# Kernel optimization log

Measured on AMD Instinct MI355X. Metric: run time of the kernel, lower is better.

## Reference

```python
import jax, jax.numpy as jnp
import numpy as np


def _conv1x1(x, w, b):
    # x: [B,C,H,W], w: [O,C], b: [O] -> [B,O,H,W]
    return jnp.einsum('bchw,oc->bohw', x, w) + b[None, :, None, None]


def setup_inputs() -> dict:
    key = jax.random.key(0)
    ks = jax.random.split(key, 5)
    B, C, H, W = 4, 256, 64, 64
    C2 = C // 2
    scale = 0.02  # keep attention logits in a sane range
    return {
        'x': jax.random.normal(ks[0], (B, C, H, W), dtype=jnp.float32),
        'w_theta': jax.random.normal(ks[1], (C2, C), dtype=jnp.float32) * scale,
        'b_theta': jnp.zeros((C2,), dtype=jnp.float32),
        'w_phi': jax.random.normal(ks[2], (C2, C), dtype=jnp.float32) * scale,
        'b_phi': jnp.zeros((C2,), dtype=jnp.float32),
        'w_g': jax.random.normal(ks[3], (C2, C), dtype=jnp.float32) * scale,
        'b_g': jnp.zeros((C2,), dtype=jnp.float32),
        'w_out': jax.random.normal(ks[4], (C, C2), dtype=jnp.float32) * scale,
        'b_out': jnp.zeros((C,), dtype=jnp.float32),
    }


def reference(x, w_theta, b_theta, w_phi, b_phi, w_g, b_g, w_out, b_out):
    B, C, H, W = x.shape
    C2 = C // 2
    N = H * W
    theta = _conv1x1(x, w_theta, b_theta).reshape(B, C2, N)  # [B,C2,N]
    phi = _conv1x1(x, w_phi, b_phi).reshape(B, C2, N)        # [B,C2,N]
    g = _conv1x1(x, w_g, b_g).reshape(B, C2, N)              # [B,C2,N]
    # non-local attention: scores[b,m,n] = theta[b,:,m] . phi[b,:,n]
    scores = jnp.einsum('bcm,bcn->bmn', theta, phi)          # [B,N,N]
    attn = jax.nn.softmax(scores, axis=-1)                   # [B,N,N]
    # output = g @ attn^T : out[b,c,m] = sum_n g[b,c,n] * attn[b,m,n]
    out = jnp.einsum('bcn,bmn->bcm', g, attn)                # [B,C2,N]
    out = out.reshape(B, C2, H, W)
    return x + _conv1x1(out, w_out, b_out)
```

## Files before the change

kernel.cpp:

```cpp
#include <hip/hip_runtime.h>
#include <hip/hip_bf16.h>

#define B_  4
#define C_  256
#define C2_ 128
#define N_  4096
#define LOG2E 1.4426950408889634f

typedef unsigned short u16;
typedef __attribute__((ext_vector_type(8))) short bf16x8;
typedef __attribute__((ext_vector_type(4))) short s16x4;
typedef __attribute__((ext_vector_type(4))) float f32x4;

static __device__ __forceinline__ u16 f2bf(float f) {
    return __builtin_bit_cast(u16, __float2bfloat16(f));
}
static __device__ __forceinline__ float bf2f(u16 u) {
    return __bfloat162float(__builtin_bit_cast(__hip_bfloat16, u));
}
static __device__ __forceinline__ bf16x8 cvt8(const float* p) {
    u16 t[8];
#pragma unroll
    for (int j = 0; j < 8; ++j) t[j] = f2bf(p[j]);
    return *(const bf16x8*)t;
}
static __device__ __forceinline__ bf16x8 lds8(const u16* p) {
    s16x4 lo = *(const s16x4*)p;
    s16x4 hi = *(const s16x4*)(p + 4);
    return __builtin_shufflevector(lo, hi, 0, 1, 2, 3, 4, 5, 6, 7);
}

__global__ __launch_bounds__(256) void prep_kernel(
    const float* __restrict__ wt, const float* __restrict__ wp,
    const float* __restrict__ wg, const float* __restrict__ wo,
    u16* __restrict__ Wb, u16* __restrict__ Wob) {
    int g = (blockIdx.x * 256 + threadIdx.x) * 8;
    const float* src;
    u16* dst;
    if (g < 3 * 32768) {
        int mat = g >> 15;
        src = (mat == 0 ? wt : mat == 1 ? wp : wg) + (g & 32767);
        dst = Wb + g;
    } else {
        src = wo + (g & 32767);
        dst = Wob + (g & 32767);
    }
    float w8[8];
    *(float4*)&w8[0] = *(const float4*)src;
    *(float4*)&w8[4] = *(const float4*)(src + 4);
    *(bf16x8*)dst = cvt8(w8);
}

#define XW 268

__global__ __launch_bounds__(256, 2) void projx_kernel(
    const float* __restrict__ x, const u16* __restrict__ Wb,
    const float* __restrict__ b_theta, const float* __restrict__ b_phi,
    const float* __restrict__ b_g,
    u16* __restrict__ Q, u16* __restrict__ K, u16* __restrict__ V) {
    __shared__ __align__(16) u16 XTs[64][XW];
    u16 (*Vt)[72] = (u16(*)[72])XTs;

    int bid = blockIdx.x;
    int h   = bid >> 8;
    int r2  = bid & 255;
    int b   = r2 >> 6;
    int n0  = (r2 & 63) * 64;
    int tid = threadIdx.x;
    int wave = tid >> 6, lane = tid & 63, quad = (lane >> 4) & 3, l16 = lane & 15;

#pragma unroll
    for (int it = 0; it < 8; ++it) {
        int idx = it * 256 + tid;
        int q = idx & 15, p = idx >> 4;
        const float* r0 = x + ((size_t)b * C_ + 2 * p) * N_ + n0 + 4 * q;
        float4 v0 = *(const float4*)r0;
        float4 v1 = *(const float4*)(r0 + N_);
        const float* f0 = (const float*)&v0;
        const float* f1 = (const float*)&v1;
#pragma unroll
        for (int j = 0; j < 4; ++j) {
            unsigned pk = (unsigned)f2bf(f0[j]) | ((unsigned)f2bf(f1[j]) << 16);
            *(unsigned*)&XTs[4 * q + j][2 * p] = pk;
        }
    }
    __syncthreads();

    bf16x8 af[8];
#pragma unroll
    for (int ks = 0; ks < 8; ++ks)
        af[ks] = lds8(&XTs[wave * 16 + l16][ks * 32 + quad * 8]);
    __syncthreads();

    const float* biases[3] = { b_theta, b_phi, b_g };

#pragma unroll
    for (int mat = 0; mat < 3; ++mat) {
        const float* bias = biases[mat];
        f32x4 acc[4];
#pragma unroll
        for (int i = 0; i < 4; ++i) acc[i] = (f32x4){0.f, 0.f, 0.f, 0.f};

#pragma unroll
        for (int ct = 0; ct < 4; ++ct) {
            const u16* wrow = Wb + mat * 32768 +
                              (size_t)(h * 64 + ct * 16 + l16) * 256 + quad * 8;
            bf16x8 bfr[8];
#pragma unroll
            for (int ks = 0; ks < 8; ++ks)
                bfr[ks] = *(const bf16x8*)(wrow + ks * 32);
#pragma unroll
            for (int ks = 0; ks < 8; ++ks)
                acc[ct] = __builtin_amdgcn_mfma_f32_16x16x32_bf16(
                    af[ks], bfr[ks], acc[ct], 0, 0, 0);
        }

        if (mat < 2) {
            u16* dst = mat == 0 ? Q : K;
            float scl = mat == 0 ? LOG2E : 1.0f;
#pragma unroll
            for (int ct = 0; ct < 4; ++ct) {
                int c2 = h * 64 + ct * 16 + l16;
                float bb = bias[c2];
#pragma unroll
                for (int r = 0; r < 4; ++r) {
                    int n = n0 + wave * 16 + quad * 4 + r;
                    dst[((size_t)b * N_ + n) * C2_ + c2] =
                        f2bf((acc[ct][r] + bb) * scl);
                }
            }
        } else {
#pragma unroll
            for (int ct = 0; ct < 4; ++ct) {
                int c2 = h * 64 + ct * 16 + l16;
                float bb = bias[c2];
#pragma unroll
                for (int r = 0; r < 4; ++r)
                    Vt[ct * 16 + l16][wave * 16 + quad * 4 + r] =
                        f2bf(acc[ct][r] + bb);
            }
        }
    }
    __syncthreads();

#pragma unroll
    for (int it = 0; it < 2; ++it) {
        int idx = it * 256 + tid;
        int row = idx >> 3, n8 = (idx & 7) * 8;
        *(uint4*)(V + ((size_t)b * C2_ + h * 64 + row) * N_ + n0 + n8) =
            *(const uint4*)&Vt[row][n8];
    }
}

#define KS_LD 140
#define VS_LD 76
#define PS_LD 68

__global__ __launch_bounds__(256, 2) void attn_kernel(
    const u16* __restrict__ Q, const u16* __restrict__ K,
    const u16* __restrict__ V, u16* __restrict__ AO,
    u16* __restrict__ Opb, float* __restrict__ lsum, int nsplit) {
    const int BM = 128, BN = 64, D = C2_;
    const int per = B_ * (N_ / BM);
    int s    = blockIdx.x / per;
    int r0   = blockIdx.x % per;
    int b    = r0 / (N_ / BM);
    int m0   = (r0 % (N_ / BM)) * BM;
    int tid  = threadIdx.x;
    int wave = tid >> 6, lane = tid & 63, quad = (lane >> 4) & 3, l16 = lane & 15;

    __shared__ __align__(16) u16 Ks[BN][KS_LD];
    __shared__ __align__(16) u16 Vs[C2_][VS_LD];
    __shared__ __align__(16) u16 Psb[4][32][PS_LD];
    u16* Ps = &Psb[wave][0][0];

    bf16x8 qf[2][4];
#pragma unroll
    for (int ms = 0; ms < 2; ++ms) {
        const u16* qp = Q + ((size_t)b * N_ + m0 + wave * 32 + ms * 16 + l16) * D;
#pragma unroll
        for (int kk = 0; kk < 4; ++kk)
            qf[ms][kk] = *(const bf16x8*)(qp + kk * 32 + quad * 8);
    }

    float l_r[2][4] = {{0.f, 0.f, 0.f, 0.f}, {0.f, 0.f, 0.f, 0.f}};
    f32x4 o_acc[2][8];
#pragma unroll
    for (int ms = 0; ms < 2; ++ms)
#pragma unroll
        for (int i = 0; i < 8; ++i) o_acc[ms][i] = (f32x4){0.f, 0.f, 0.f, 0.f};

    const int tiles = N_ / BN;
    const int base = tiles / nsplit, rem = tiles % nsplit;
    const int t0 = s * base + (s < rem ? s : rem);
    const int cnt = base + (s < rem ? 1 : 0);
    const int nt0 = t0 * BN, nt1 = (t0 + cnt) * BN;

    for (int nt = nt0; nt < nt1; nt += BN) {
        const u16* kp = K + ((size_t)b * N_ + nt) * D;
#pragma unroll
        for (int it = 0; it < 4; ++it) {
            int idx = it * 256 + tid;
            int row = idx >> 4, col = (idx & 15) * 8;
            uint4 raw = *(const uint4*)(kp + row * D + col);
            *(uint2*)&Ks[row][col]     = make_uint2(raw.x, raw.y);
            *(uint2*)&Ks[row][col + 4] = make_uint2(raw.z, raw.w);
        }
#pragma unroll
        for (int it = 0; it < 4; ++it) {
            int idx = it * 256 + tid;
            int row = idx >> 3, col = (idx & 7) * 8;
            uint4 raw = *(const uint4*)(V + ((size_t)b * C2_ + row) * N_ + nt + col);
            *(uint2*)&Vs[row][col]     = make_uint2(raw.x, raw.y);
            *(uint2*)&Vs[row][col + 4] = make_uint2(raw.z, raw.w);
        }
        __syncthreads();

#pragma unroll
        for (int nn = 0; nn < 4; ++nn) {
            f32x4 a0 = (f32x4){0.f, 0.f, 0.f, 0.f};
            f32x4 a1 = (f32x4){0.f, 0.f, 0.f, 0.f};
#pragma unroll
            for (int kk = 0; kk < 4; ++kk) {
                bf16x8 kf = lds8(&Ks[nn * 16 + l16][kk * 32 + quad * 8]);
                a0 = __builtin_amdgcn_mfma_f32_16x16x32_bf16(qf[0][kk], kf, a0, 0, 0, 0);
                a1 = __builtin_amdgcn_mfma_f32_16x16x32_bf16(qf[1][kk], kf, a1, 0, 0, 0);
            }
#pragma unroll
            for (int r = 0; r < 4; ++r) {
                float p0 = __builtin_amdgcn_exp2f(a0[r]);
                float p1 = __builtin_amdgcn_exp2f(a1[r]);
                l_r[0][r] += p0;
                l_r[1][r] += p1;
                Ps[(quad * 4 + r) * PS_LD + nn * 16 + l16]        = f2bf(p0);
                Ps[(16 + quad * 4 + r) * PS_LD + nn * 16 + l16]   = f2bf(p1);
            }
        }

#pragma unroll
        for (int ks = 0; ks < 2; ++ks) {
            bf16x8 pf0 = lds8(Ps + l16 * PS_LD + ks * 32 + quad * 8);
            bf16x8 pf1 = lds8(Ps + (16 + l16) * PS_LD + ks * 32 + quad * 8);
#pragma unroll
            for (int cs = 0; cs < 8; ++cs) {
                bf16x8 vf = lds8(&Vs[cs * 16 + l16][ks * 32 + quad * 8]);
                o_acc[0][cs] = __builtin_amdgcn_mfma_f32_16x16x32_bf16(pf0, vf, o_acc[0][cs], 0, 0, 0);
                o_acc[1][cs] = __builtin_amdgcn_mfma_f32_16x16x32_bf16(pf1, vf, o_acc[1][cs], 0, 0, 0);
            }
        }
        __syncthreads();
    }

#pragma unroll
    for (int ms = 0; ms < 2; ++ms)
#pragma unroll
        for (int r = 0; r < 4; ++r) {
            l_r[ms][r] += __shfl_xor(l_r[ms][r], 1);
            l_r[ms][r] += __shfl_xor(l_r[ms][r], 2);
            l_r[ms][r] += __shfl_xor(l_r[ms][r], 4);
            l_r[ms][r] += __shfl_xor(l_r[ms][r], 8);
        }

    if (Opb) {
#pragma unroll
        for (int ms = 0; ms < 2; ++ms) {
#pragma unroll
            for (int cs = 0; cs < 8; ++cs)
#pragma unroll
                for (int r = 0; r < 4; ++r) {
                    size_t row = (size_t)s * (B_ * N_) + (size_t)b * N_ +
                                 m0 + wave * 32 + ms * 16 + quad * 4 + r;
                    Opb[row * C2_ + cs * 16 + l16] = f2bf(o_acc[ms][cs][r]);
                }
            if (l16 == 0)
#pragma unroll
                for (int r = 0; r < 4; ++r) {
                    size_t row = (size_t)s * (B_ * N_) + (size_t)b * N_ +
                                 m0 + wave * 32 + ms * 16 + quad * 4 + r;
                    lsum[row] = l_r[ms][r];
                }
        }
    } else {
#pragma unroll
        for (int ms = 0; ms < 2; ++ms)
#pragma unroll
            for (int cs = 0; cs < 8; ++cs)
#pragma unroll
                for (int r = 0; r < 4; ++r) {
                    float v = o_acc[ms][cs][r] / l_r[ms][r];
                    AO[((size_t)b * N_ + m0 + wave * 32 + ms * 16 + quad * 4 + r) * C2_ +
                       cs * 16 + l16] = f2bf(v);
                }
    }
}

#define OW 140

__global__ __launch_bounds__(256, 4) void outproj_kernel(
    const float* __restrict__ x, const u16* __restrict__ Opb,
    const float* __restrict__ lsum, const u16* __restrict__ AO,
    const u16* __restrict__ Wob, const float* __restrict__ b_out,
    float* __restrict__ y, int nsplit) {
    __shared__ __align__(16) u16 As[64][OW];
    __shared__ float Ls[64];
    int bid = blockIdx.x;
    int per_b = (C_ / 64) * (N_ / 64);
    int b   = bid / per_b;
    int rem = bid % per_b;
    int c0  = (rem / (N_ / 64)) * 64;
    int n0  = (rem % (N_ / 64)) * 64;
    int tid = threadIdx.x;
    int wave = tid >> 6, lane = tid & 63, quad = (lane >> 4) & 3, l16 = lane & 15;

    bf16x8 af[4];
#pragma unroll
    for (int kk = 0; kk < 4; ++kk)
        af[kk] = *(const bf16x8*)(Wob + (size_t)(c0 + wave * 16 + l16) * C2_ +
                                  kk * 32 + quad * 8);

    if (nsplit > 1) {
        if (tid < 64) {
            float L = 0.f;
            for (int s = 0; s < nsplit; ++s)
                L += lsum[(size_t)s * (B_ * N_) + (size_t)b * N_ + n0 + tid];
            Ls[tid] = 1.f / L;
        }
        __syncthreads();
#pragma unroll
        for (int it = 0; it < 4; ++it) {
            int idx = it * 256 + tid;
            int n = idx >> 4, c8 = (idx & 15) * 8;
            float a[8] = {0.f, 0.f, 0.f, 0.f, 0.f, 0.f, 0.f, 0.f};
            for (int s = 0; s < nsplit; ++s) {
                const u16* op = Opb +
                    ((size_t)s * (B_ * N_) + (size_t)b * N_ + n0 + n) * C2_ + c8;
                uint4 raw = *(const uint4*)op;
                const u16* rp = (const u16*)&raw;
#pragma unroll
                for (int j = 0; j < 8; ++j) a[j] += bf2f(rp[j]);
            }
            float inv = Ls[n];
            u16 o[8];
#pragma unroll
            for (int j = 0; j < 8; ++j) o[j] = f2bf(a[j] * inv);
            *(s16x4*)&As[n][c8]     = *(const s16x4*)&o[0];
            *(s16x4*)&As[n][c8 + 4] = *(const s16x4*)&o[4];
        }
    } else {
#pragma unroll
        for (int it = 0; it < 4; ++it) {
            int idx = it * 256 + tid;
            int n = idx >> 4, c8 = (idx & 15) * 8;
            uint4 raw = *(const uint4*)(AO + ((size_t)b * N_ + n0 + n) * C2_ + c8);
            *(uint2*)&As[n][c8]     = make_uint2(raw.x, raw.y);
            *(uint2*)&As[n][c8 + 4] = make_uint2(raw.z, raw.w);
        }
    }
    __syncthreads();

    f32x4 acc[4];
#pragma unroll
    for (int i = 0; i < 4; ++i) acc[i] = (f32x4){0.f, 0.f, 0.f, 0.f};

#pragma unroll
    for (int nn = 0; nn < 4; ++nn)
#pragma unroll
        for (int kk = 0; kk < 4; ++kk) {
            bf16x8 bf = lds8(&As[nn * 16 + l16][kk * 32 + quad * 8]);
            acc[nn] = __builtin_amdgcn_mfma_f32_16x16x32_bf16(af[kk], bf, acc[nn], 0, 0, 0);
        }

    int cw = c0 + wave * 16;
    float bo[4];
#pragma unroll
    for (int r = 0; r < 4; ++r) bo[r] = b_out[cw + quad * 4 + r];

#pragma unroll
    for (int nn = 0; nn < 4; ++nn)
#pragma unroll
        for (int r = 0; r < 4; ++r) {
            int c = cw + quad * 4 + r;
            size_t off = ((size_t)b * C_ + c) * N_ + n0 + nn * 16 + l16;
            y[off] = x[off] + bo[r] + acc[nn][r];
        }
}

extern "C" void kernel_launch(void* const* d_in, const int* in_sizes, int n_in,
                              void* d_out, int out_size, void* d_ws, size_t ws_size,
                              hipStream_t stream) {
    const float* x       = (const float*)d_in[0];
    const float* w_theta = (const float*)d_in[1];
    const float* b_theta = (const float*)d_in[2];
    const float* w_phi   = (const float*)d_in[3];
    const float* b_phi   = (const float*)d_in[4];
    const float* w_g     = (const float*)d_in[5];
    const float* b_g     = (const float*)d_in[6];
    const float* w_out   = (const float*)d_in[7];
    const float* b_out   = (const float*)d_in[8];
    float* y = (float*)d_out;

    const size_t SZ = (size_t)B_ * N_ * C2_;
    u16* Q   = (u16*)d_ws;
    u16* K   = Q + SZ;
    u16* V   = K + SZ;
    u16* Wb  = V + SZ;
    u16* Wob = Wb + 3 * 32768;
    char* dyn = (char*)(Wob + 32768);
    size_t fixedB = (3 * SZ + 4 * 32768) * 2;

    size_t perS = SZ * 2 + (size_t)B_ * N_ * 4;

    int S;
    if      (ws_size >= fixedB + 4 * perS) S = 4;
    else if (ws_size >= fixedB + 2 * perS) S = 2;
    else                                   S = 1;

    u16*   AO  = (u16*)dyn;
    u16*   Opb = nullptr;
    float* ls  = nullptr;
    if (S > 1) {
        Opb = (u16*)dyn;
        ls  = (float*)(Opb + (size_t)S * SZ);
    }

    prep_kernel<<<64, 256, 0, stream>>>(w_theta, w_phi, w_g, w_out, Wb, Wob);
    projx_kernel<<<B_ * (N_ / 64) * 2, 256, 0, stream>>>(
        x, Wb, b_theta, b_phi, b_g, Q, K, V);
    attn_kernel<<<B_ * (N_ / 128) * S, 256, 0, stream>>>(Q, K, V, AO, Opb, ls, S);
    outproj_kernel<<<B_ * (C_ / 64) * (N_ / 64), 256, 0, stream>>>(
        x, Opb, ls, AO, Wob, b_out, y, S);
}
```

Before: 168.9 us.

## Split projection into transpose+GEMM kernels, separate split combine, widen LDS loads

Adds a separate kernel that transposes x into bf16 [B,N,C], so the projection kernel reads A-fragments straight from global memory and each block handles one matrix and half its channels. The split-K combine moves out of outproj into its own kernel, and outproj now reads AO directly from global memory instead of staging it through LDS. In the attention kernel, LDS padding shrinks to +8, staging uses single 16-byte stores and reads, and all score MFMAs finish before the exp phase. The goal is more parallelism and fewer redundant x reads. In exchange it adds an extra bf16 copy of x, two more kernel launches, and possible LDS bank conflicts from the new padding.

```diff
diff --git a/kernel.cpp b/kernel.cpp
--- a/kernel.cpp
+++ b/kernel.cpp
@@ -9,7 +9,6 @@
 
 typedef unsigned short u16;
 typedef __attribute__((ext_vector_type(8))) short bf16x8;
-typedef __attribute__((ext_vector_type(4))) short s16x4;
 typedef __attribute__((ext_vector_type(4))) float f32x4;
 
 static __device__ __forceinline__ u16 f2bf(float f) {
@@ -23,11 +22,6 @@
 #pragma unroll
     for (int j = 0; j < 8; ++j) t[j] = f2bf(p[j]);
     return *(const bf16x8*)t;
-}
-static __device__ __forceinline__ bf16x8 lds8(const u16* p) {
-    s16x4 lo = *(const s16x4*)p;
-    s16x4 hi = *(const s16x4*)(p + 4);
-    return __builtin_shufflevector(lo, hi, 0, 1, 2, 3, 4, 5, 6, 7);
 }
 
 __global__ __launch_bounds__(256) void prep_kernel(
@@ -51,29 +45,18 @@
     *(bf16x8*)dst = cvt8(w8);
 }
 
-#define XW 268
-
-__global__ __launch_bounds__(256, 2) void projx_kernel(
-    const float* __restrict__ x, const u16* __restrict__ Wb,
-    const float* __restrict__ b_theta, const float* __restrict__ b_phi,
-    const float* __restrict__ b_g,
-    u16* __restrict__ Q, u16* __restrict__ K, u16* __restrict__ V) {
-    __shared__ __align__(16) u16 XTs[64][XW];
-    u16 (*Vt)[72] = (u16(*)[72])XTs;
-
+__global__ __launch_bounds__(256) void xpose_kernel(
+    const float* __restrict__ x, u16* __restrict__ XT) {
+    __shared__ __align__(16) u16 Ts[64][72];
     int bid = blockIdx.x;
-    int h   = bid >> 8;
-    int r2  = bid & 255;
-    int b   = r2 >> 6;
-    int n0  = (r2 & 63) * 64;
+    int b = bid >> 8, rem = bid & 255;
+    int c0 = (rem >> 6) * 64, n0 = (rem & 63) * 64;
     int tid = threadIdx.x;
-    int wave = tid >> 6, lane = tid & 63, quad = (lane >> 4) & 3, l16 = lane & 15;
-
-#pragma unroll
-    for (int it = 0; it < 8; ++it) {
+#pragma unroll
+    for (int it = 0; it < 2; ++it) {
         int idx = it * 256 + tid;
         int q = idx & 15, p = idx >> 4;
-        const float* r0 = x + ((size_t)b * C_ + 2 * p) * N_ + n0 + 4 * q;
+        const float* r0 = x + ((size_t)b * C_ + c0 + 2 * p) * N_ + n0 + 4 * q;
         float4 v0 = *(const float4*)r0;
         float4 v1 = *(const float4*)(r0 + N_);
         const float* f0 = (const float*)&v0;
@@ -81,80 +64,94 @@
 #pragma unroll
         for (int j = 0; j < 4; ++j) {
             unsigned pk = (unsigned)f2bf(f0[j]) | ((unsigned)f2bf(f1[j]) << 16);
-            *(unsigned*)&XTs[4 * q + j][2 * p] = pk;
+            *(unsigned*)&Ts[4 * q + j][2 * p] = pk;
         }
     }
     __syncthreads();
-
-    bf16x8 af[8];
-#pragma unroll
-    for (int ks = 0; ks < 8; ++ks)
-        af[ks] = lds8(&XTs[wave * 16 + l16][ks * 32 + quad * 8]);
-    __syncthreads();
-
-    const float* biases[3] = { b_theta, b_phi, b_g };
-
-#pragma unroll
-    for (int mat = 0; mat < 3; ++mat) {
-        const float* bias = biases[mat];
-        f32x4 acc[4];
-#pragma unroll
-        for (int i = 0; i < 4; ++i) acc[i] = (f32x4){0.f, 0.f, 0.f, 0.f};
-
-#pragma unroll
-        for (int ct = 0; ct < 4; ++ct) {
-            const u16* wrow = Wb + mat * 32768 +
-                              (size_t)(h * 64 + ct * 16 + l16) * 256 + quad * 8;
-            bf16x8 bfr[8];
-#pragma unroll
-            for (int ks = 0; ks < 8; ++ks)
-                bfr[ks] = *(const bf16x8*)(wrow + ks * 32);
-#pragma unroll
-            for (int ks = 0; ks < 8; ++ks)
-                acc[ct] = __builtin_amdgcn_mfma_f32_16x16x32_bf16(
-                    af[ks], bfr[ks], acc[ct], 0, 0, 0);
-        }
-
-        if (mat < 2) {
-            u16* dst = mat == 0 ? Q : K;
-            float scl = mat == 0 ? LOG2E : 1.0f;
-#pragma unroll
-            for (int ct = 0; ct < 4; ++ct) {
-                int c2 = h * 64 + ct * 16 + l16;
-                float bb = bias[c2];
-#pragma unroll
-                for (int r = 0; r < 4; ++r) {
-                    int n = n0 + wave * 16 + quad * 4 + r;
-                    dst[((size_t)b * N_ + n) * C2_ + c2] =
-                        f2bf((acc[ct][r] + bb) * scl);
-                }
-            }
-        } else {
-#pragma unroll
-            for (int ct = 0; ct < 4; ++ct) {
-                int c2 = h * 64 + ct * 16 + l16;
-                float bb = bias[c2];
-#pragma unroll
-                for (int r = 0; r < 4; ++r)
-                    Vt[ct * 16 + l16][wave * 16 + quad * 4 + r] =
-                        f2bf(acc[ct][r] + bb);
-            }
-        }
-    }
-    __syncthreads();
-
 #pragma unroll
     for (int it = 0; it < 2; ++it) {
         int idx = it * 256 + tid;
-        int row = idx >> 3, n8 = (idx & 7) * 8;
-        *(uint4*)(V + ((size_t)b * C2_ + h * 64 + row) * N_ + n0 + n8) =
-            *(const uint4*)&Vt[row][n8];
-    }
-}
-
-#define KS_LD 140
-#define VS_LD 76
-#define PS_LD 68
+        int row = idx >> 3, ch = (idx & 7) * 8;
+        *(uint4*)(XT + ((size_t)(b * N_ + n0 + row)) * C_ + c0 + ch) =
+            *(const uint4*)&Ts[row][ch];
+    }
+}
+
+__global__ __launch_bounds__(256, 2) void projx_kernel(
+    const u16* __restrict__ XT, const u16* __restrict__ Wb,
+    const float* __restrict__ b_theta, const float* __restrict__ b_phi,
+    const float* __restrict__ b_g,
+    u16* __restrict__ Q, u16* __restrict__ K, u16* __restrict__ V) {
+    __shared__ __align__(16) u16 Vt[64][72];
+
+    int bid = blockIdx.x;
+    int nt  = bid & 255;
+    int cm  = bid >> 8;
+    int mat = cm >> 1, h = cm & 1;
+    int b   = nt >> 6;
+    int n0  = (nt & 63) * 64;
+    int tid = threadIdx.x;
+    int wave = tid >> 6, lane = tid & 63, quad = (lane >> 4) & 3, l16 = lane & 15;
+
+    const u16* xrow = XT + ((size_t)(b * N_ + n0 + wave * 16 + l16)) * C_ + quad * 8;
+    bf16x8 af[8];
+#pragma unroll
+    for (int ks = 0; ks < 8; ++ks)
+        af[ks] = *(const bf16x8*)(xrow + ks * 32);
+
+    const float* bias = mat == 0 ? b_theta : mat == 1 ? b_phi : b_g;
+
+    f32x4 acc[4];
+#pragma unroll
+    for (int i = 0; i < 4; ++i) acc[i] = (f32x4){0.f, 0.f, 0.f, 0.f};
+
+#pragma unroll
+    for (int ct = 0; ct < 4; ++ct) {
+        const u16* wrow = Wb + mat * 32768 +
+                          (size_t)(h * 64 + ct * 16 + l16) * 256 + quad * 8;
+        bf16x8 bfr[8];
+#pragma unroll
+        for (int ks = 0; ks < 8; ++ks)
+            bfr[ks] = *(const bf16x8*)(wrow + ks * 32);
+#pragma unroll
+        for (int ks = 0; ks < 8; ++ks)
+            acc[ct] = __builtin_amdgcn_mfma_f32_16x16x32_bf16(
+                af[ks], bfr[ks], acc[ct], 0, 0, 0);
+    }
+
+    if (mat < 2) {
+        u16* dst = mat == 0 ? Q : K;
+        float scl = mat == 0 ? LOG2E : 1.0f;
+#pragma unroll
+        for (int ct = 0; ct < 4; ++ct) {
+            int c2 = h * 64 + ct * 16 + l16;
+            float bb = bias[c2];
+#pragma unroll
+            for (int r = 0; r < 4; ++r) {
+                int n = n0 + wave * 16 + quad * 4 + r;
+                dst[((size_t)b * N_ + n) * C2_ + c2] =
+                    f2bf((acc[ct][r] + bb) * scl);
+            }
+        }
+    } else {
+#pragma unroll
+        for (int ct = 0; ct < 4; ++ct) {
+            int c2l = ct * 16 + l16;
+            float bb = bias[h * 64 + c2l];
+#pragma unroll
+            for (int r = 0; r < 4; ++r)
+                Vt[c2l][wave * 16 + quad * 4 + r] = f2bf(acc[ct][r] + bb);
+        }
+        __syncthreads();
+#pragma unroll
+        for (int it = 0; it < 2; ++it) {
+            int idx = it * 256 + tid;
+            int row = idx >> 3, n8 = (idx & 7) * 8;
+            *(uint4*)(V + ((size_t)b * C2_ + h * 64 + row) * N_ + n0 + n8) =
+                *(const uint4*)&Vt[row][n8];
+        }
+    }
+}
 
 __global__ __launch_bounds__(256, 2) void attn_kernel(
     const u16* __restrict__ Q, const u16* __restrict__ K,
@@ -169,9 +166,9 @@
     int tid  = threadIdx.x;
     int wave = tid >> 6, lane = tid & 63, quad = (lane >> 4) & 3, l16 = lane & 15;
 
-    __shared__ __align__(16) u16 Ks[BN][KS_LD];
-    __shared__ __align__(16) u16 Vs[C2_][VS_LD];
-    __shared__ __align__(16) u16 Psb[4][32][PS_LD];
+    __shared__ __align__(16) u16 Ks[BN][D + 8];
+    __shared__ __align__(16) u16 Vs[D][BN + 8];
+    __shared__ __align__(16) u16 Psb[4][32][BN + 8];
     u16* Ps = &Psb[wave][0][0];
 
     bf16x8 qf[2][4];
@@ -202,48 +199,50 @@
         for (int it = 0; it < 4; ++it) {
             int idx = it * 256 + tid;
             int row = idx >> 4, col = (idx & 15) * 8;
-            uint4 raw = *(const uint4*)(kp + row * D + col);
-            *(uint2*)&Ks[row][col]     = make_uint2(raw.x, raw.y);
-            *(uint2*)&Ks[row][col + 4] = make_uint2(raw.z, raw.w);
+            *(uint4*)&Ks[row][col] = *(const uint4*)(kp + row * D + col);
         }
 #pragma unroll
         for (int it = 0; it < 4; ++it) {
             int idx = it * 256 + tid;
             int row = idx >> 3, col = (idx & 7) * 8;
-            uint4 raw = *(const uint4*)(V + ((size_t)b * C2_ + row) * N_ + nt + col);
-            *(uint2*)&Vs[row][col]     = make_uint2(raw.x, raw.y);
-            *(uint2*)&Vs[row][col + 4] = make_uint2(raw.z, raw.w);
+            *(uint4*)&Vs[row][col] =
+                *(const uint4*)(V + ((size_t)b * C2_ + row) * N_ + nt + col);
         }
         __syncthreads();
 
+        f32x4 sc[2][4];
 #pragma unroll
         for (int nn = 0; nn < 4; ++nn) {
             f32x4 a0 = (f32x4){0.f, 0.f, 0.f, 0.f};
             f32x4 a1 = (f32x4){0.f, 0.f, 0.f, 0.f};
 #pragma unroll
             for (int kk = 0; kk < 4; ++kk) {
-                bf16x8 kf = lds8(&Ks[nn * 16 + l16][kk * 32 + quad * 8]);
+                bf16x8 kf = *(const bf16x8*)&Ks[nn * 16 + l16][kk * 32 + quad * 8];
                 a0 = __builtin_amdgcn_mfma_f32_16x16x32_bf16(qf[0][kk], kf, a0, 0, 0, 0);
                 a1 = __builtin_amdgcn_mfma_f32_16x16x32_bf16(qf[1][kk], kf, a1, 0, 0, 0);
             }
-#pragma unroll
-            for (int r = 0; r < 4; ++r) {
-                float p0 = __builtin_amdgcn_exp2f(a0[r]);
-                float p1 = __builtin_amdgcn_exp2f(a1[r]);
-                l_r[0][r] += p0;
-                l_r[1][r] += p1;
-                Ps[(quad * 4 + r) * PS_LD + nn * 16 + l16]        = f2bf(p0);
-                Ps[(16 + quad * 4 + r) * PS_LD + nn * 16 + l16]   = f2bf(p1);
-            }
-        }
+            sc[0][nn] = a0;
+            sc[1][nn] = a1;
+        }
+
+#pragma unroll
+        for (int ms = 0; ms < 2; ++ms)
+#pragma unroll
+            for (int nn = 0; nn < 4; ++nn)
+#pragma unroll
+                for (int r = 0; r < 4; ++r) {
+                    float p = __builtin_amdgcn_exp2f(sc[ms][nn][r]);
+                    l_r[ms][r] += p;
+                    Ps[(ms * 16 + quad * 4 + r) * (BN + 8) + nn * 16 + l16] = f2bf(p);
+                }
 
 #pragma unroll
         for (int ks = 0; ks < 2; ++ks) {
-            bf16x8 pf0 = lds8(Ps + l16 * PS_LD + ks * 32 + quad * 8);
-            bf16x8 pf1 = lds8(Ps + (16 + l16) * PS_LD + ks * 32 + quad * 8);
+            bf16x8 pf0 = *(const bf16x8*)&Ps[(l16) * (BN + 8) + ks * 32 + quad * 8];
+            bf16x8 pf1 = *(const bf16x8*)&Ps[(16 + l16) * (BN + 8) + ks * 32 + quad * 8];
 #pragma unroll
             for (int cs = 0; cs < 8; ++cs) {
-                bf16x8 vf = lds8(&Vs[cs * 16 + l16][ks * 32 + quad * 8]);
+                bf16x8 vf = *(const bf16x8*)&Vs[cs * 16 + l16][ks * 32 + quad * 8];
                 o_acc[0][cs] = __builtin_amdgcn_mfma_f32_16x16x32_bf16(pf0, vf, o_acc[0][cs], 0, 0, 0);
                 o_acc[1][cs] = __builtin_amdgcn_mfma_f32_16x16x32_bf16(pf1, vf, o_acc[1][cs], 0, 0, 0);
             }
@@ -294,21 +293,38 @@
     }
 }
 
-#define OW 140
-
-__global__ __launch_bounds__(256, 4) void outproj_kernel(
-    const float* __restrict__ x, const u16* __restrict__ Opb,
-    const float* __restrict__ lsum, const u16* __restrict__ AO,
+__global__ __launch_bounds__(256) void combine_kernel(
+    const u16* __restrict__ Opb, const float* __restrict__ lsum,
+    u16* __restrict__ AO, int nsplit) {
+    int gid = blockIdx.x * 256 + threadIdx.x;
+    int row = gid >> 4, c8 = (gid & 15) * 8;
+    float L = 0.f;
+    for (int s = 0; s < nsplit; ++s)
+        L += lsum[(size_t)s * (B_ * N_) + row];
+    float inv = 1.f / L;
+    float a[8] = {0.f, 0.f, 0.f, 0.f, 0.f, 0.f, 0.f, 0.f};
+    for (int s = 0; s < nsplit; ++s) {
+        const u16* op = Opb + ((size_t)s * (B_ * N_) + row) * C2_ + c8;
+        uint4 raw = *(const uint4*)op;
+        const u16* rp = (const u16*)&raw;
+#pragma unroll
+        for (int j = 0; j < 8; ++j) a[j] += bf2f(rp[j]);
+    }
+    u16 o[8];
+#pragma unroll
+    for (int j = 0; j < 8; ++j) o[j] = f2bf(a[j] * inv);
+    *(uint4*)(AO + (size_t)row * C2_ + c8) = *(const uint4*)o;
+}
+
+__global__ __launch_bounds__(256, 2) void outproj_kernel(
+    const float* __restrict__ x, const u16* __restrict__ AO,
     const u16* __restrict__ Wob, const float* __restrict__ b_out,
-    float* __restrict__ y, int nsplit) {
-    __shared__ __align__(16) u16 As[64][OW];
-    __shared__ float Ls[64];
+    float* __restrict__ y) {
     int bid = blockIdx.x;
-    int per_b = (C_ / 64) * (N_ / 64);
-    int b   = bid / per_b;
-    int rem = bid % per_b;
-    int c0  = (rem / (N_ / 64)) * 64;
-    int n0  = (rem % (N_ / 64)) * 64;
+    int b   = bid >> 8;
+    int rem = bid & 255;
+    int c0  = (rem >> 6) * 64;
+    int n0  = (rem & 63) * 64;
     int tid = threadIdx.x;
     int wave = tid >> 6, lane = tid & 63, quad = (lane >> 4) & 3, l16 = lane & 15;
 
@@ -318,57 +334,21 @@
         af[kk] = *(const bf16x8*)(Wob + (size_t)(c0 + wave * 16 + l16) * C2_ +
                                   kk * 32 + quad * 8);
 
-    if (nsplit > 1) {
-        if (tid < 64) {
-            float L = 0.f;
-            for (int s = 0; s < nsplit; ++s)
-                L += lsum[(size_t)s * (B_ * N_) + (size_t)b * N_ + n0 + tid];
-            Ls[tid] = 1.f / L;
-        }
-        __syncthreads();
-#pragma unroll
-        for (int it = 0; it < 4; ++it) {
-            int idx = it * 256 + tid;
-            int n = idx >> 4, c8 = (idx & 15) * 8;
-            float a[8] = {0.f, 0.f, 0.f, 0.f, 0.f, 0.f, 0.f, 0.f};
-            for (int s = 0; s < nsplit; ++s) {
-                const u16* op = Opb +
-                    ((size_t)s * (B_ * N_) + (size_t)b * N_ + n0 + n) * C2_ + c8;
-                uint4 raw = *(const uint4*)op;
-                const u16* rp = (const u16*)&raw;
-#pragma unroll
-                for (int j = 0; j < 8; ++j) a[j] += bf2f(rp[j]);
-            }
-            float inv = Ls[n];
-            u16 o[8];
-#pragma unroll
-            for (int j = 0; j < 8; ++j) o[j] = f2bf(a[j] * inv);
-            *(s16x4*)&As[n][c8]     = *(const s16x4*)&o[0];
-            *(s16x4*)&As[n][c8 + 4] = *(const s16x4*)&o[4];
-        }
-    } else {
-#pragma unroll
-        for (int it = 0; it < 4; ++it) {
-            int idx = it * 256 + tid;
-            int n = idx >> 4, c8 = (idx & 15) * 8;
-            uint4 raw = *(const uint4*)(AO + ((size_t)b * N_ + n0 + n) * C2_ + c8);
-            *(uint2*)&As[n][c8]     = make_uint2(raw.x, raw.y);
-            *(uint2*)&As[n][c8 + 4] = make_uint2(raw.z, raw.w);
-        }
-    }
-    __syncthreads();
-
     f32x4 acc[4];
 #pragma unroll
     for (int i = 0; i < 4; ++i) acc[i] = (f32x4){0.f, 0.f, 0.f, 0.f};
 
 #pragma unroll
-    for (int nn = 0; nn < 4; ++nn)
-#pragma unroll
-        for (int kk = 0; kk < 4; ++kk) {
-            bf16x8 bf = lds8(&As[nn * 16 + l16][kk * 32 + quad * 8]);
-            acc[nn] = __builtin_amdgcn_mfma_f32_16x16x32_bf16(af[kk], bf, acc[nn], 0, 0, 0);
-        }
+    for (int nn = 0; nn < 4; ++nn) {
+        const u16* arow = AO + ((size_t)b * N_ + n0 + nn * 16 + l16) * C2_ + quad * 8;
+        bf16x8 bfr[4];
+#pragma unroll
+        for (int kk = 0; kk < 4; ++kk)
+            bfr[kk] = *(const bf16x8*)(arow + kk * 32);
+#pragma unroll
+        for (int kk = 0; kk < 4; ++kk)
+            acc[nn] = __builtin_amdgcn_mfma_f32_16x16x32_bf16(af[kk], bfr[kk], acc[nn], 0, 0, 0);
+    }
 
     int cw = c0 + wave * 16;
     float bo[4];
@@ -399,14 +379,17 @@
     const float* b_out   = (const float*)d_in[8];
     float* y = (float*)d_out;
 
-    const size_t SZ = (size_t)B_ * N_ * C2_;
+    const size_t SZ  = (size_t)B_ * N_ * C2_;
+    const size_t XTE = (size_t)B_ * N_ * C_;
     u16* Q   = (u16*)d_ws;
     u16* K   = Q + SZ;
     u16* V   = K + SZ;
     u16* Wb  = V + SZ;
     u16* Wob = Wb + 3 * 32768;
-    char* dyn = (char*)(Wob + 32768);
-    size_t fixedB = (3 * SZ + 4 * 32768) * 2;
+    u16* XT  = Wob + 32768;
+    u16* AO  = XT + XTE;
+    char* dyn = (char*)(AO + SZ);
+    size_t fixedB = (4 * SZ + 4 * 32768 + XTE) * 2;
 
     size_t perS = SZ * 2 + (size_t)B_ * N_ * 4;
 
@@ -415,7 +398,6 @@
     else if (ws_size >= fixedB + 2 * perS) S = 2;
     else                                   S = 1;
 
-    u16*   AO  = (u16*)dyn;
     u16*   Opb = nullptr;
     float* ls  = nullptr;
     if (S > 1) {
@@ -424,9 +406,11 @@
     }
 
     prep_kernel<<<64, 256, 0, stream>>>(w_theta, w_phi, w_g, w_out, Wb, Wob);
-    projx_kernel<<<B_ * (N_ / 64) * 2, 256, 0, stream>>>(
-        x, Wb, b_theta, b_phi, b_g, Q, K, V);
+    xpose_kernel<<<1024, 256, 0, stream>>>(x, XT);
+    projx_kernel<<<1536, 256, 0, stream>>>(
+        XT, Wb, b_theta, b_phi, b_g, Q, K, V);
     attn_kernel<<<B_ * (N_ / 128) * S, 256, 0, stream>>>(Q, K, V, AO, Opb, ls, S);
-    outproj_kernel<<<B_ * (C_ / 64) * (N_ / 64), 256, 0, stream>>>(
-        x, Opb, ls, AO, Wob, b_out, y, S);
-}
+    if (S > 1)
+        combine_kernel<<<1024, 256, 0, stream>>>(Opb, ls, AO, S);
+    outproj_kernel<<<1024, 256, 0, stream>>>(x, AO, Wob, b_out, y);
+}
```

New measurement: 181.6 us. +7.5%, slower.
